# Kernel tuning notes

Measured on AMD Instinct MI355X. Metric: run time of the kernel, lower is better.

Reference implementation:

```python
import jax, jax.numpy as jnp
import numpy as np

N = 50000   # nodes
C = 128     # num_channels
E = 800000  # edges (before self loops)
P = 8192    # pos/neg pairs
L = 2       # num_layers
NEG_SLOPE = 0.2  # GATv2Conv default negative_slope


def setup_inputs() -> dict:
    key = jax.random.key(0)
    ks = jax.random.split(key, 10)
    x = jax.random.normal(ks[0], (N, C), dtype=jnp.float32)
    edge_index = jax.random.randint(ks[1], (2, E), 0, N)
    true_pairs = jax.random.randint(ks[2], (P, 2), 0, N)
    false_pairs = jax.random.randint(ks[3], (P, 2), 0, N)
    s = 1.0 / np.sqrt(C)
    # GATv2Conv params per layer (heads=1, share_weights=False): lin_l, lin_r, att, bias
    Wl = jax.random.normal(ks[4], (L, C, C), dtype=jnp.float32) * s
    Wr = jax.random.normal(ks[5], (L, C, C), dtype=jnp.float32) * s
    att_w = jax.random.normal(ks[6], (L, C), dtype=jnp.float32) * s
    bias = jnp.zeros((L, C), dtype=jnp.float32)
    # ConcatAndLogisticScorer classifier: Linear(2C,C) -> ReLU -> Linear(C,1) -> Sigmoid
    W1 = jax.random.normal(ks[7], (2 * C, C), dtype=jnp.float32) * (1.0 / np.sqrt(2 * C))
    b1 = jnp.zeros((C,), dtype=jnp.float32)
    W2 = jax.random.normal(ks[8], (C, 1), dtype=jnp.float32) * s
    b2 = jnp.zeros((1,), dtype=jnp.float32)
    return dict(x=x, edge_index=edge_index, true_pairs=true_pairs, false_pairs=false_pairs,
                Wl=Wl, Wr=Wr, att_w=att_w, bias=bias, W1=W1, b1=b1, W2=W2, b2=b2)


def _gatv2_layer(h, src, dst, Wl, Wr, a, b):
    # single-head GATv2: e_ij = a^T LeakyReLU(Wl h_j + Wr h_i); softmax over incoming edges of i
    n = h.shape[0]
    xl = h @ Wl  # [N,C] (source transform, also the message value)
    xr = h @ Wr  # [N,C] (target transform)
    z = xl[src] + xr[dst]                       # [E,C]
    z = jnp.where(z >= 0, z, NEG_SLOPE * z)     # leaky_relu
    e = z @ a                                   # [E]
    emax = jax.ops.segment_max(e, dst, num_segments=n)
    p = jnp.exp(e - emax[dst])
    denom = jax.ops.segment_sum(p, dst, num_segments=n)
    alpha = p / denom[dst]                      # edge softmax per dst node
    out = jax.ops.segment_sum(alpha[:, None] * xl[src], dst, num_segments=n)
    return out + b


def _gnn_and_score(x, src, dst, Wl, Wr, att_w, bias, W1, b1, W2, b2, true_pairs, false_pairs):
    h = x
    n_layers = Wl.shape[0]
    for l in range(n_layers):
        h = _gatv2_layer(h, src, dst, Wl[l], Wr[l], att_w[l], bias[l])
        if l < n_layers - 1:  # BasicGNN: activation between layers, not after last
            h = jax.nn.relu(h)
    pos = jnp.concatenate([h[true_pairs[:, 0]], h[true_pairs[:, 1]]], axis=-1)   # [P,2C]
    neg = jnp.concatenate([h[false_pairs[:, 0]], h[false_pairs[:, 1]]], axis=-1)  # [P,2C]
    v = jnp.concatenate([pos, neg], axis=0)  # [2P,2C]
    hid = jax.nn.relu(v @ W1 + b1)
    probs = jax.nn.sigmoid(hid @ W2 + b2)    # [2P,1]
    return pos, neg, probs


def reference(x, edge_index, true_pairs, false_pairs, Wl, Wr, att_w, bias, W1, b1, W2, b2):
    n = x.shape[0]
    loop = jnp.arange(n)  # GATv2Conv add_self_loops=True
    src = jnp.concatenate([edge_index[0], loop])
    dst = jnp.concatenate([edge_index[1], loop])
    pos, neg, probs = _gnn_and_score(x, src, dst, Wl, Wr, att_w, bias, W1, b1, W2, b2,
                                     true_pairs, false_pairs)
    npos = pos.shape[0]
    labels = jnp.concatenate([jnp.ones((npos, 1), jnp.float32),
                              jnp.zeros((probs.shape[0] - npos, 1), jnp.float32)], axis=0)
    pcl = jnp.clip(probs, 1e-7, 1.0 - 1e-7)  # BCELoss log clamping
    loss = -jnp.mean(labels * jnp.log(pcl) + (1.0 - labels) * jnp.log1p(-pcl))
    return pos, neg, probs, loss
```

## Files before the change

kernel.cpp:

```cpp
#include <hip/hip_runtime.h>
#include <math.h>

#define C 128
#define SCAN_B 1024

typedef unsigned short ushort_t;
typedef short short8 __attribute__((ext_vector_type(8)));
typedef float floatx4 __attribute__((ext_vector_type(4)));
typedef float fx2 __attribute__((ext_vector_type(2)));

__device__ __forceinline__ ushort_t f2bf(float x) {
  unsigned u = __float_as_uint(x);
  unsigned r = (u + 0x7FFFu + ((u >> 16) & 1u)) >> 16;
  return (ushort_t)r;
}
__device__ __forceinline__ fx2 bf2f2(unsigned u) {
  fx2 r;
  r.x = __uint_as_float(u << 16);
  r.y = __uint_as_float(u & 0xFFFF0000u);
  return r;
}


__global__ void k_init_prep(int* __restrict__ deg, int* __restrict__ mark,
                            float* __restrict__ lossacc,
                            unsigned* __restrict__ done_cnt, int* __restrict__ ncnt, int n,
                            const float* __restrict__ Wl, const float* __restrict__ Wr,
                            const float* __restrict__ W1,
                            ushort_t* __restrict__ wcat, ushort_t* __restrict__ w1t) {
  int idx = blockIdx.x * blockDim.x + threadIdx.x;
  if (idx < n) { deg[idx] = 0; mark[idx] = 0; }
  if (idx == 0) { lossacc[0] = 0.f; done_cnt[0] = 0u; ncnt[0] = 0; }
  const int NCAT = 2 * 256 * 128;
  if (idx < NCAT) {
    int l = idx >> 15;
    int rem = idx & 32767;
    int nn = rem >> 7;
    int k = rem & 127;
    float v = (nn < 128) ? Wl[l * C * C + k * C + nn] : Wr[l * C * C + k * C + (nn - 128)];
    wcat[idx] = f2bf(v);
  } else if (idx < NCAT + 128 * 256) {
    int j = idx - NCAT;
    int nn = j >> 8;
    int k = j & 255;
    w1t[j] = f2bf(W1[k * C + nn]);
  }
}


__global__ void k_conv_hist(const float* __restrict__ x, ushort_t* __restrict__ xb, int total4,
                            const int* __restrict__ ei, int* __restrict__ deg,
                            int* __restrict__ pos, int E, int ET,
                            const int* __restrict__ tp, const int* __restrict__ fp, int npair2,
                            int* __restrict__ mark, int* __restrict__ nlist, int* __restrict__ ncnt) {
  int i = blockIdx.x * blockDim.x + threadIdx.x;
  if (i < total4) {
    float4 v = ((const float4*)x)[i];
    ushort4 s;
    s.x = f2bf(v.x); s.y = f2bf(v.y); s.z = f2bf(v.z); s.w = f2bf(v.w);
    ((ushort4*)xb)[i] = s;
  }
  if (i < ET) {
    int d = (i < E) ? ei[E + i] : (i - E);
    pos[i] = atomicAdd(&deg[d], 1);
  }
  if (i < 2 * npair2) {
    int node = (i < npair2) ? tp[i] : fp[i - npair2];
    if (atomicExch(&mark[node], 1) == 0) {
      int k = atomicAdd(ncnt, 1);
      nlist[k] = node;
    }
  }
}


__global__ void scan_block(const int* __restrict__ deg, int* __restrict__ row_ptr,
                           int* __restrict__ bsums, int n) {
  __shared__ int sh[SCAN_B];
  int tid = threadIdx.x;
  int i = blockIdx.x * SCAN_B + tid;
  int v = (i < n) ? deg[i] : 0;
  sh[tid] = v;
  __syncthreads();
  #pragma unroll
  for (int off = 1; off < SCAN_B; off <<= 1) {
    int t = (tid >= off) ? sh[tid - off] : 0;
    __syncthreads();
    sh[tid] += t;
    __syncthreads();
  }
  if (i < n) row_ptr[i] = sh[tid] - v;
  if (tid == SCAN_B - 1) bsums[blockIdx.x] = sh[tid];
}

__global__ void scan_sums(int* __restrict__ bsums, int nb, int* __restrict__ row_ptr, int n) {
  int lane = threadIdx.x;
  int v = (lane < nb) ? bsums[lane] : 0;
  int orig = v;
  #pragma unroll
  for (int off = 1; off < 64; off <<= 1) {
    int t = __shfl_up(v, off);
    if (lane >= off) v += t;
  }
  if (lane < nb) bsums[lane] = v - orig;
  if (lane == nb - 1) row_ptr[n] = orig;
}


__device__ __forceinline__ void gemm_body(
    const ushort_t* __restrict__ A, const ushort_t* __restrict__ Bt,
    int M, int K,
    ushort_t* __restrict__ outb0, ushort_t* __restrict__ outb1,
    float* __restrict__ outf, const float* __restrict__ bias, int do_relu,
    int bx, int by) {
  int tid = threadIdx.x;
  int wave = tid >> 6, lane = tid & 63;
  int wm = (wave >> 1) * 64, wn = (wave & 1) * 64;
  int m_base = bx * 128 + wm;
  int lrow = lane & 15, lkg = lane >> 4;

  floatx4 acc[4][4];
  #pragma unroll
  for (int mi = 0; mi < 4; mi++)
    #pragma unroll
    for (int ni = 0; ni < 4; ni++)
      acc[mi][ni] = (floatx4){0.f, 0.f, 0.f, 0.f};

  const int ksteps = K >> 5;
  for (int ks = 0; ks < ksteps; ks++) {
    int koff = ks * 32 + lkg * 8;
    short8 af[4], bfr[4];
    #pragma unroll
    for (int mi = 0; mi < 4; mi++) {
      int gm = m_base + mi * 16 + lrow;
      gm = (gm < M) ? gm : (M - 1);
      af[mi] = *(const short8*)&A[(size_t)gm * K + koff];
    }
    #pragma unroll
    for (int ni = 0; ni < 4; ni++) {
      int gn = by * 128 + wn + ni * 16 + lrow;
      bfr[ni] = *(const short8*)&Bt[(size_t)gn * K + koff];
    }
    #pragma unroll
    for (int mi = 0; mi < 4; mi++)
      #pragma unroll
      for (int ni = 0; ni < 4; ni++)
        acc[mi][ni] = __builtin_amdgcn_mfma_f32_16x16x32_bf16(af[mi], bfr[ni], acc[mi][ni], 0, 0, 0);
  }

  ushort_t* outb = (by == 0) ? outb0 : outb1;
  #pragma unroll
  for (int mi = 0; mi < 4; mi++) {
    #pragma unroll
    for (int r = 0; r < 4; r++) {
      int gm = m_base + mi * 16 + lkg * 4 + r;
      if (gm >= M) continue;
      #pragma unroll
      for (int ni = 0; ni < 4; ni++) {
        int nl = wn + ni * 16 + lrow;
        float v = acc[mi][ni][r];
        if (outf) {
          if (bias) v += bias[nl];
          if (do_relu) v = fmaxf(v, 0.f);
          outf[(size_t)gm * 128 + nl] = v;
        } else {
          outb[(size_t)gm * 128 + nl] = f2bf(v);
        }
      }
    }
  }
}

__global__ __launch_bounds__(256) void gemm_mfma(
    const ushort_t* __restrict__ A, const ushort_t* __restrict__ Bt,
    int M, int K,
    ushort_t* __restrict__ outb0, ushort_t* __restrict__ outb1,
    float* __restrict__ outf, const float* __restrict__ bias, int do_relu) {
  gemm_body(A, Bt, M, K, outb0, outb1, outf, bias, do_relu, blockIdx.x, blockIdx.y);
}


__global__ __launch_bounds__(256) void k_gemm_scatter(
    const ushort_t* __restrict__ A, const ushort_t* __restrict__ Bt,
    int M, int K,
    ushort_t* __restrict__ outb0, ushort_t* __restrict__ outb1, int gb,
    const int* __restrict__ ei, const int* __restrict__ row_ptr,
    const int* __restrict__ bsums, const int* __restrict__ pos,
    int* __restrict__ col, int E, int ET, int ETp) {
  int bx = blockIdx.x;
  if (bx < gb) {
    gemm_body(A, Bt, M, K, outb0, outb1, nullptr, nullptr, 0, bx, blockIdx.y);
  } else {
    int chunk = (bx - gb) * 2 + blockIdx.y;
    int e = chunk * 256 + threadIdx.x;
    if (e < ET) {
      int s = (e < E) ? ei[e] : (e - E);
      int d = (e < E) ? ei[E + e] : (e - E);
      col[row_ptr[d] + bsums[d >> 10] + pos[e]] = s;
    } else if (e < ETp) {
      col[e] = 0;
    }
  }
}


__global__ __launch_bounds__(256) void gat_aggregate(
    const ushort_t* __restrict__ xl, const ushort_t* __restrict__ xr,
    const int* __restrict__ row_ptr, const int* __restrict__ bsums,
    const int* __restrict__ col,
    const float* __restrict__ att, const float* __restrict__ bias,
    float* __restrict__ houtf, ushort_t* __restrict__ houtb,
    const int* __restrict__ nlist, const int* __restrict__ ncnt,
    int n, int do_relu) {
  int gwid = (int)((blockIdx.x * (size_t)blockDim.x + threadIdx.x) >> 6);
  int lane = threadIdx.x & 63;
  int wid;
  if (nlist) {
    if (gwid >= ncnt[0]) return;
    wid = nlist[gwid];
  } else {
    if (gwid >= n) return;
    wid = gwid;
  }
  int g = lane >> 4, p = lane & 15;
  int c0 = p * 8;
  const size_t i = wid;

  fx2 xri[4], av[4];
  {
    uint4 ur = *(const uint4*)&xr[i * C + c0];
    xri[0] = bf2f2(ur.x); xri[1] = bf2f2(ur.y);
    xri[2] = bf2f2(ur.z); xri[3] = bf2f2(ur.w);
    float4 a0 = *(const float4*)&att[c0];
    float4 a1 = *(const float4*)&att[c0 + 4];
    const float L2E = 1.44269504088896f;
    av[0] = (fx2){a0.x * L2E, a0.y * L2E}; av[1] = (fx2){a0.z * L2E, a0.w * L2E};
    av[2] = (fx2){a1.x * L2E, a1.y * L2E}; av[3] = (fx2){a1.z * L2E, a1.w * L2E};
  }

  int beg = row_ptr[wid] + bsums[wid >> 10];
  int end = row_ptr[wid + 1] + bsums[(wid + 1) >> 10];
  float denom = 0.f;
  fx2 acc[4];
  #pragma unroll
  for (int q = 0; q < 4; q++) acc[q] = (fx2){0.f, 0.f};

  for (int base = beg; base < end; base += 8) {
    int e0 = base + g;
    int e1 = e0 + 4;
    int j0 = col[e0];
    int j1 = col[e1];
    uint4 r0 = *(const uint4*)&xl[((size_t)j0 << 7) + c0];
    uint4 r1 = *(const uint4*)&xl[((size_t)j1 << 7) + c0];
    fx2 x0[4], x1[4];
    x0[0] = bf2f2(r0.x); x0[1] = bf2f2(r0.y); x0[2] = bf2f2(r0.z); x0[3] = bf2f2(r0.w);
    x1[0] = bf2f2(r1.x); x1[1] = bf2f2(r1.y); x1[2] = bf2f2(r1.z); x1[3] = bf2f2(r1.w);

    fx2 d0 = (fx2){0.f, 0.f}, d1 = (fx2){0.f, 0.f};
    #pragma unroll
    for (int q = 0; q < 4; q++) {
      fx2 z0 = x0[q] + xri[q];
      fx2 z1 = x1[q] + xri[q];
      z0 = __builtin_elementwise_max(z0, z0 * 0.2f);
      z1 = __builtin_elementwise_max(z1, z1 * 0.2f);
      d0 = __builtin_elementwise_fma(z0, av[q], d0);
      d1 = __builtin_elementwise_fma(z1, av[q], d1);
    }
    float p0 = d0.x + d0.y;
    float p1 = d1.x + d1.y;
    #pragma unroll
    for (int off = 1; off <= 8; off <<= 1) {
      p0 += __shfl_xor(p0, off);
      p1 += __shfl_xor(p1, off);
    }
    float pe0 = (e0 < end) ? __builtin_amdgcn_exp2f(p0) : 0.f;
    float pe1 = (e1 < end) ? __builtin_amdgcn_exp2f(p1) : 0.f;
    denom += pe0 + pe1;
    fx2 v0 = (fx2){pe0, pe0}, v1 = (fx2){pe1, pe1};
    #pragma unroll
    for (int q = 0; q < 4; q++) {
      acc[q] = __builtin_elementwise_fma(v0, x0[q], acc[q]);
      acc[q] = __builtin_elementwise_fma(v1, x1[q], acc[q]);
    }
  }

  #pragma unroll
  for (int off = 16; off <= 32; off <<= 1) {
    denom += __shfl_xor(denom, off);
    #pragma unroll
    for (int q = 0; q < 4; q++) {
      acc[q].x += __shfl_xor(acc[q].x, off);
      acc[q].y += __shfl_xor(acc[q].y, off);
    }
  }

  if (g == 0) {
    float inv = 1.f / denom;
    float4 b0 = *(const float4*)&bias[c0];
    float4 b1 = *(const float4*)&bias[c0 + 4];
    float o[8];
    o[0] = acc[0].x*inv + b0.x; o[1] = acc[0].y*inv + b0.y;
    o[2] = acc[1].x*inv + b0.z; o[3] = acc[1].y*inv + b0.w;
    o[4] = acc[2].x*inv + b1.x; o[5] = acc[2].y*inv + b1.y;
    o[6] = acc[3].x*inv + b1.z; o[7] = acc[3].y*inv + b1.w;
    if (do_relu) {
      #pragma unroll
      for (int c = 0; c < 8; c++) o[c] = fmaxf(o[c], 0.f);
    }
    if (houtf) {
      *(float4*)&houtf[i * C + c0]     = make_float4(o[0], o[1], o[2], o[3]);
      *(float4*)&houtf[i * C + c0 + 4] = make_float4(o[4], o[5], o[6], o[7]);
    } else {
      short8 s;
      #pragma unroll
      for (int c = 0; c < 8; c++) s[c] = (short)f2bf(o[c]);
      *(short8*)&houtb[i * C + c0] = s;
    }
  }
}


__global__ __launch_bounds__(256) void gemm_scorer(
    const float* __restrict__ h, const int* __restrict__ tp, const int* __restrict__ fp,
    const ushort_t* __restrict__ w1t, float* __restrict__ out_pos,
    const float* __restrict__ b1, const float* __restrict__ W2,
    const float* __restrict__ b2, float* __restrict__ probs_out,
    float* __restrict__ lossacc, unsigned* __restrict__ done_cnt,
    float* __restrict__ out_loss, int P2, int P) {
  __shared__ float lhalf[2][128];
  __shared__ float red[128];
  int tid = threadIdx.x;
  int wave = tid >> 6, lane = tid & 63;
  int wm = (wave >> 1) * 64, wn = (wave & 1) * 64;
  int m_base = blockIdx.x * 128 + wm;
  int lrow = lane & 15, lkg = lane >> 4;
  int half = P2 >> 1;
  bool emit = (wn == 0);

  int n0[4], n1[4];
  #pragma unroll
  for (int mi = 0; mi < 4; mi++) {
    int gm = m_base + mi * 16 + lrow;
    const int* pr = (gm < half) ? &tp[(size_t)gm * 2] : &fp[(size_t)(gm - half) * 2];
    n0[mi] = pr[0];
    n1[mi] = pr[1];
  }

  floatx4 acc[4][4];
  #pragma unroll
  for (int mi = 0; mi < 4; mi++)
    #pragma unroll
    for (int ni = 0; ni < 4; ni++)
      acc[mi][ni] = (floatx4){0.f, 0.f, 0.f, 0.f};

  #pragma unroll
  for (int ks = 0; ks < 8; ks++) {
    int koff = ks * 32 + lkg * 8;
    int chan = koff & 127;
    short8 af[4], bfr[4];
    #pragma unroll
    for (int mi = 0; mi < 4; mi++) {
      int node = (ks < 4) ? n0[mi] : n1[mi];
      const float* src = &h[(size_t)node * C + chan];
      float4 lo = *(const float4*)src;
      float4 hi = *(const float4*)(src + 4);
      if (emit) {
        int gm = m_base + mi * 16 + lrow;
        *(float4*)&out_pos[(size_t)gm * 256 + koff]     = lo;
        *(float4*)&out_pos[(size_t)gm * 256 + koff + 4] = hi;
      }
      short8 a;
      a[0] = (short)f2bf(lo.x); a[1] = (short)f2bf(lo.y);
      a[2] = (short)f2bf(lo.z); a[3] = (short)f2bf(lo.w);
      a[4] = (short)f2bf(hi.x); a[5] = (short)f2bf(hi.y);
      a[6] = (short)f2bf(hi.z); a[7] = (short)f2bf(hi.w);
      af[mi] = a;
    }
    #pragma unroll
    for (int ni = 0; ni < 4; ni++) {
      int gn = wn + ni * 16 + lrow;
      bfr[ni] = *(const short8*)&w1t[(size_t)gn * 256 + koff];
    }
    #pragma unroll
    for (int mi = 0; mi < 4; mi++)
      #pragma unroll
      for (int ni = 0; ni < 4; ni++)
        acc[mi][ni] = __builtin_amdgcn_mfma_f32_16x16x32_bf16(af[mi], bfr[ni], acc[mi][ni], 0, 0, 0);
  }

  float b1v[4], w2v[4];
  #pragma unroll
  for (int ni = 0; ni < 4; ni++) {
    int nl = wn + ni * 16 + lrow;
    b1v[ni] = b1[nl];
    w2v[ni] = W2[nl];
  }
  #pragma unroll
  for (int mi = 0; mi < 4; mi++) {
    #pragma unroll
    for (int r = 0; r < 4; r++) {
      float ps = 0.f;
      #pragma unroll
      for (int ni = 0; ni < 4; ni++) {
        float v = fmaxf(acc[mi][ni][r] + b1v[ni], 0.f);
        ps = fmaf(v, w2v[ni], ps);
      }
      #pragma unroll
      for (int off = 1; off <= 8; off <<= 1)
        ps += __shfl_xor(ps, off);
      if (lrow == 0)
        lhalf[wn ? 1 : 0][wm + mi * 16 + lkg * 4 + r] = ps;
    }
  }
  __syncthreads();

  float term = 0.f;
  if (tid < 128) {
    int gr = blockIdx.x * 128 + tid;
    float s = lhalf[0][tid] + lhalf[1][tid] + b2[0];
    float pv = 1.f / (1.f + expf(-s));
    probs_out[gr] = pv;
    float pcl = fminf(fmaxf(pv, 1e-7f), 1.f - 1e-7f);
    term = (gr < P) ? logf(pcl) : log1pf(-pcl);
    red[tid] = term;
  }
  __syncthreads();
  if (tid < 64) red[tid] += red[tid + 64];
  __syncthreads();
  if (tid < 32) red[tid] += red[tid + 32];
  __syncthreads();
  if (tid == 0) {
    float s = 0.f;
    #pragma unroll
    for (int k = 0; k < 32; k++) s += red[k];
    atomicAdd(lossacc, s);
    __threadfence();
    unsigned prev = atomicAdd(done_cnt, 1u);
    if (prev == gridDim.x - 1) {
      float total = atomicAdd(lossacc, 0.f);
      out_loss[0] = -total / (float)P2;
    }
  }
}


extern "C" void kernel_launch(void* const* d_in, const int* in_sizes, int n_in,
                              void* d_out, int out_size, void* d_ws, size_t ws_size,
                              hipStream_t stream) {
  const float* x    = (const float*)d_in[0];
  const int*   ei   = (const int*)d_in[1];
  const int*   tp   = (const int*)d_in[2];
  const int*   fp   = (const int*)d_in[3];
  const float* Wl   = (const float*)d_in[4];
  const float* Wr   = (const float*)d_in[5];
  const float* att  = (const float*)d_in[6];
  const float* bias = (const float*)d_in[7];
  const float* W1   = (const float*)d_in[8];
  const float* b1   = (const float*)d_in[9];
  const float* W2   = (const float*)d_in[10];
  const float* b2   = (const float*)d_in[11];

  int N  = in_sizes[0] / C;
  int E  = in_sizes[1] / 2;
  int P  = in_sizes[2] / 2;
  int ET = E + N;
  int ETp = ET + 8;
  int P2 = 2 * P;
  int npair2 = 2 * P;
  int nb = (N + SCAN_B - 1) / SCAN_B;

  float* out       = (float*)d_out;
  float* out_pos   = out;
  float* out_probs = out + (size_t)P2 * 2 * C;
  float* out_loss  = out_probs + P2;

  char* w = (char*)d_ws;
  size_t NCb2 = (size_t)N * C * 2;
  ushort_t* x_bf  = (ushort_t*)w;  w += NCb2;
  ushort_t* xl_bf = (ushort_t*)w;  w += NCb2;
  ushort_t* xr_bf = (ushort_t*)w;  w += NCb2;
  ushort_t* h1_bf = (ushort_t*)w;  w += NCb2;
  float* h1f = (float*)w;          w += (size_t)N * C * 4;
  ushort_t* wcat = (ushort_t*)w;   w += (size_t)2 * 256 * 128 * 2;
  ushort_t* w1t  = (ushort_t*)w;   w += (size_t)128 * 256 * 2;
  int* deg     = (int*)w;  w += (size_t)N * 4;
  int* mark    = (int*)w;  w += (size_t)N * 4;
  int* nlist   = (int*)w;  w += (size_t)(2 * npair2) * 4;
  int* row_ptr = (int*)w;  w += (size_t)(N + 1) * 4 + 12;
  int* pos     = (int*)w;  w += (size_t)ET * 4;
  int* col     = (int*)w;  w += (size_t)ETp * 4;
  int* bsums   = (int*)w;  w += (size_t)(nb + 1) * 4 + 8;
  float* lossacc = (float*)w;  w += 16;
  unsigned* done_cnt = (unsigned*)w;  w += 16;
  int* ncnt    = (int*)w;

  const int tB = 256;
  int total4 = N * C / 4;

  k_init_prep<<<384, tB, 0, stream>>>(deg, mark, lossacc, done_cnt, ncnt, N, Wl, Wr, W1, wcat, w1t);
  k_conv_hist<<<(total4 + tB - 1) / tB, tB, 0, stream>>>(
      x, x_bf, total4, ei, deg, pos, E, ET, tp, fp, npair2, mark, nlist, ncnt);

  scan_block<<<nb, SCAN_B, 0, stream>>>(deg, row_ptr, bsums, N);
  scan_sums<<<1, 64, 0, stream>>>(bsums, nb, row_ptr, N);

  int gblk = (N + 127) / 128;
  int schunks = (ETp + tB - 1) / tB;
  int sxtra = (schunks + 1) / 2;

  k_gemm_scatter<<<dim3(gblk + sxtra, 2), tB, 0, stream>>>(
      x_bf, wcat, N, C, xl_bf, xr_bf, gblk, ei, row_ptr, bsums, pos, col, E, ET, ETp);

  gat_aggregate<<<(N * 64 + tB - 1) / tB, tB, 0, stream>>>(
      xl_bf, xr_bf, row_ptr, bsums, col, att, bias, nullptr, h1_bf,
      nullptr, nullptr, N, 1);

  gemm_mfma<<<dim3(gblk, 2), tB, 0, stream>>>(
      h1_bf, wcat + (size_t)256 * 128, N, C, xl_bf, xr_bf, nullptr, nullptr, 0);
  int lblk = (2 * npair2 * 64 + tB - 1) / tB;
  gat_aggregate<<<lblk, tB, 0, stream>>>(
      xl_bf, xr_bf, row_ptr, bsums, col, att + C, bias + C, h1f, nullptr,
      nlist, ncnt, N, 0);

  gemm_scorer<<<P2 / 128, tB, 0, stream>>>(
      h1f, tp, fp, w1t, out_pos, b1, W2, b2, out_probs,
      lossacc, done_cnt, out_loss, P2, P);
}
```

Before: 205.5 us.

## Fuse x bf16 conversion into GEMM, single-pass scan, restrict layer-2 xr rows

Removes the separate x-to-bf16 conversion pass; the first GEMM now loads fp32 x and converts it in registers. The two scan kernels become one decoupled scan in which the last block to finish computes the block offsets. The layer-2 target-transform GEMM (by==1) now computes xr only for the nodes the final aggregation needs, gathered through nlist/ncnt, which cuts that half of the GEMM's work. In exchange the GEMM reads twice the bytes for A in layer 1, and the scan relies on atomics and fences for cross-block ordering.

After: 219.1 us. 6.6% more time.

```diff
diff --git a/kernel.cpp b/kernel.cpp
--- a/kernel.cpp
+++ b/kernel.cpp
@@ -2,7 +2,6 @@
 #include <math.h>
 
 #define C 128
-#define SCAN_B 1024
 
 typedef unsigned short ushort_t;
 typedef short short8 __attribute__((ext_vector_type(8)));
@@ -24,13 +23,14 @@
 
 __global__ void k_init_prep(int* __restrict__ deg, int* __restrict__ mark,
                             float* __restrict__ lossacc,
-                            unsigned* __restrict__ done_cnt, int* __restrict__ ncnt, int n,
+                            unsigned* __restrict__ done_cnt, int* __restrict__ ncnt,
+                            unsigned* __restrict__ scnt, int n,
                             const float* __restrict__ Wl, const float* __restrict__ Wr,
                             const float* __restrict__ W1,
                             ushort_t* __restrict__ wcat, ushort_t* __restrict__ w1t) {
   int idx = blockIdx.x * blockDim.x + threadIdx.x;
   if (idx < n) { deg[idx] = 0; mark[idx] = 0; }
-  if (idx == 0) { lossacc[0] = 0.f; done_cnt[0] = 0u; ncnt[0] = 0; }
+  if (idx == 0) { lossacc[0] = 0.f; done_cnt[0] = 0u; ncnt[0] = 0; scnt[0] = 0u; }
   const int NCAT = 2 * 256 * 128;
   if (idx < NCAT) {
     int l = idx >> 15;
@@ -48,18 +48,11 @@
 }
 
 
-__global__ void k_conv_hist(const float* __restrict__ x, ushort_t* __restrict__ xb, int total4,
-                            const int* __restrict__ ei, int* __restrict__ deg,
-                            int* __restrict__ pos, int E, int ET,
-                            const int* __restrict__ tp, const int* __restrict__ fp, int npair2,
-                            int* __restrict__ mark, int* __restrict__ nlist, int* __restrict__ ncnt) {
+__global__ void k_hist(const int* __restrict__ ei, int* __restrict__ deg,
+                       int* __restrict__ pos, int E, int ET,
+                       const int* __restrict__ tp, const int* __restrict__ fp, int npair2,
+                       int* __restrict__ mark, int* __restrict__ nlist, int* __restrict__ ncnt) {
   int i = blockIdx.x * blockDim.x + threadIdx.x;
-  if (i < total4) {
-    float4 v = ((const float4*)x)[i];
-    ushort4 s;
-    s.x = f2bf(v.x); s.y = f2bf(v.y); s.z = f2bf(v.z); s.w = f2bf(v.w);
-    ((ushort4*)xb)[i] = s;
-  }
   if (i < ET) {
     int d = (i < E) ? ei[E + i] : (i - E);
     pos[i] = atomicAdd(&deg[d], 1);
@@ -74,45 +67,67 @@
 }
 
 
-__global__ void scan_block(const int* __restrict__ deg, int* __restrict__ row_ptr,
-                           int* __restrict__ bsums, int n) {
-  __shared__ int sh[SCAN_B];
+__global__ __launch_bounds__(1024) void scan_fast(
+    const int* __restrict__ deg, int* __restrict__ row_ptr, int* __restrict__ bsums,
+    unsigned* __restrict__ scnt, int n, int nb, int nblocks) {
+  __shared__ int wsum[16];
+  __shared__ int lastflag;
   int tid = threadIdx.x;
-  int i = blockIdx.x * SCAN_B + tid;
+  int w = tid >> 6, lane = tid & 63;
+  int i = blockIdx.x * 1024 + tid;
   int v = (i < n) ? deg[i] : 0;
-  sh[tid] = v;
-  __syncthreads();
-  #pragma unroll
-  for (int off = 1; off < SCAN_B; off <<= 1) {
-    int t = (tid >= off) ? sh[tid - off] : 0;
-    __syncthreads();
-    sh[tid] += t;
-    __syncthreads();
-  }
-  if (i < n) row_ptr[i] = sh[tid] - v;
-  if (tid == SCAN_B - 1) bsums[blockIdx.x] = sh[tid];
-}
-
-__global__ void scan_sums(int* __restrict__ bsums, int nb, int* __restrict__ row_ptr, int n) {
-  int lane = threadIdx.x;
-  int v = (lane < nb) ? bsums[lane] : 0;
-  int orig = v;
-  #pragma unroll
-  for (int off = 1; off < 64; off <<= 1) {
-    int t = __shfl_up(v, off);
-    if (lane >= off) v += t;
-  }
-  if (lane < nb) bsums[lane] = v - orig;
-  if (lane == nb - 1) row_ptr[n] = orig;
+  int s = v;
+  #pragma unroll
+  for (int off = 1; off <= 32; off <<= 1) {
+    int t = __shfl_up(s, off);
+    if (lane >= off) s += t;
+  }
+  if (lane == 63) wsum[w] = s;
+  __syncthreads();
+  if (w == 0) {
+    int ws = (lane < 16) ? wsum[lane] : 0;
+    #pragma unroll
+    for (int off = 1; off <= 8; off <<= 1) {
+      int t = __shfl_up(ws, off);
+      if (lane >= off) ws += t;
+    }
+    if (lane < 16) wsum[lane] = ws;
+  }
+  __syncthreads();
+  int woff = (w == 0) ? 0 : wsum[w - 1];
+  if (i < n) row_ptr[i] = woff + s - v;
+  if (tid == 0) atomicExch(&bsums[blockIdx.x], wsum[15]);
+  __threadfence();
+  if (tid == 0) {
+    unsigned t = atomicAdd(scnt, 1u);
+    lastflag = (t == (unsigned)(nblocks - 1)) ? 1 : 0;
+  }
+  __syncthreads();
+  if (lastflag && w == 0) {
+    __threadfence();
+    int bv = (lane < nb) ? atomicAdd(&bsums[lane], 0) : 0;
+    int orig = bv;
+    #pragma unroll
+    for (int off = 1; off <= 32; off <<= 1) {
+      int t = __shfl_up(bv, off);
+      if (lane >= off) bv += t;
+    }
+    if (lane < nb) bsums[lane] = bv - orig;
+    if (lane == nb - 1) row_ptr[n] = orig;
+  }
 }
 
 
 __device__ __forceinline__ void gemm_body(
-    const ushort_t* __restrict__ A, const ushort_t* __restrict__ Bt,
-    int M, int K,
+    const ushort_t* __restrict__ A, const float* __restrict__ Af,
+    const ushort_t* __restrict__ Bt, int M, int K,
     ushort_t* __restrict__ outb0, ushort_t* __restrict__ outb1,
-    float* __restrict__ outf, const float* __restrict__ bias, int do_relu,
+    const int* __restrict__ rowmap, const int* __restrict__ rowcnt,
     int bx, int by) {
+  bool restricted = (by == 1) && (rowmap != nullptr);
+  int nc = restricted ? rowcnt[0] : 0;
+  if (restricted && bx * 128 >= nc) return;
+
   int tid = threadIdx.x;
   int wave = tid >> 6, lane = tid & 63;
   int wm = (wave >> 1) * 64, wn = (wave & 1) * 64;
@@ -133,8 +148,26 @@
     #pragma unroll
     for (int mi = 0; mi < 4; mi++) {
       int gm = m_base + mi * 16 + lrow;
-      gm = (gm < M) ? gm : (M - 1);
-      af[mi] = *(const short8*)&A[(size_t)gm * K + koff];
+      int arow;
+      if (restricted) {
+        int cg = (gm < nc) ? gm : (nc - 1);
+        arow = rowmap[cg];
+      } else {
+        arow = (gm < M) ? gm : (M - 1);
+      }
+      if (Af) {
+        const float* src = &Af[(size_t)arow * K + koff];
+        float4 lo = *(const float4*)src;
+        float4 hi = *(const float4*)(src + 4);
+        short8 a;
+        a[0] = (short)f2bf(lo.x); a[1] = (short)f2bf(lo.y);
+        a[2] = (short)f2bf(lo.z); a[3] = (short)f2bf(lo.w);
+        a[4] = (short)f2bf(hi.x); a[5] = (short)f2bf(hi.y);
+        a[6] = (short)f2bf(hi.z); a[7] = (short)f2bf(hi.w);
+        af[mi] = a;
+      } else {
+        af[mi] = *(const short8*)&A[(size_t)arow * K + koff];
+      }
     }
     #pragma unroll
     for (int ni = 0; ni < 4; ni++) {
@@ -154,18 +187,18 @@
     #pragma unroll
     for (int r = 0; r < 4; r++) {
       int gm = m_base + mi * 16 + lkg * 4 + r;
-      if (gm >= M) continue;
+      int orow;
+      if (restricted) {
+        if (gm >= nc) continue;
+        orow = rowmap[gm];
+      } else {
+        if (gm >= M) continue;
+        orow = gm;
+      }
       #pragma unroll
       for (int ni = 0; ni < 4; ni++) {
         int nl = wn + ni * 16 + lrow;
-        float v = acc[mi][ni][r];
-        if (outf) {
-          if (bias) v += bias[nl];
-          if (do_relu) v = fmaxf(v, 0.f);
-          outf[(size_t)gm * 128 + nl] = v;
-        } else {
-          outb[(size_t)gm * 128 + nl] = f2bf(v);
-        }
+        outb[(size_t)orow * 128 + nl] = f2bf(acc[mi][ni][r]);
       }
     }
   }
@@ -175,13 +208,13 @@
     const ushort_t* __restrict__ A, const ushort_t* __restrict__ Bt,
     int M, int K,
     ushort_t* __restrict__ outb0, ushort_t* __restrict__ outb1,
-    float* __restrict__ outf, const float* __restrict__ bias, int do_relu) {
-  gemm_body(A, Bt, M, K, outb0, outb1, outf, bias, do_relu, blockIdx.x, blockIdx.y);
+    const int* __restrict__ rowmap, const int* __restrict__ rowcnt) {
+  gemm_body(A, nullptr, Bt, M, K, outb0, outb1, rowmap, rowcnt, blockIdx.x, blockIdx.y);
 }
 
 
 __global__ __launch_bounds__(256) void k_gemm_scatter(
-    const ushort_t* __restrict__ A, const ushort_t* __restrict__ Bt,
+    const float* __restrict__ x, const ushort_t* __restrict__ Bt,
     int M, int K,
     ushort_t* __restrict__ outb0, ushort_t* __restrict__ outb1, int gb,
     const int* __restrict__ ei, const int* __restrict__ row_ptr,
@@ -189,7 +222,7 @@
     int* __restrict__ col, int E, int ET, int ETp) {
   int bx = blockIdx.x;
   if (bx < gb) {
-    gemm_body(A, Bt, M, K, outb0, outb1, nullptr, nullptr, 0, bx, blockIdx.y);
+    gemm_body(nullptr, x, Bt, M, K, outb0, outb1, nullptr, nullptr, bx, blockIdx.y);
   } else {
     int chunk = (bx - gb) * 2 + blockIdx.y;
     int e = chunk * 256 + threadIdx.x;
@@ -467,7 +500,7 @@
   int ETp = ET + 8;
   int P2 = 2 * P;
   int npair2 = 2 * P;
-  int nb = (N + SCAN_B - 1) / SCAN_B;
+  int nb = (N + 1023) / 1024;
 
   float* out       = (float*)d_out;
   float* out_pos   = out;
@@ -476,7 +509,6 @@
 
   char* w = (char*)d_ws;
   size_t NCb2 = (size_t)N * C * 2;
-  ushort_t* x_bf  = (ushort_t*)w;  w += NCb2;
   ushort_t* xl_bf = (ushort_t*)w;  w += NCb2;
   ushort_t* xr_bf = (ushort_t*)w;  w += NCb2;
   ushort_t* h1_bf = (ushort_t*)w;  w += NCb2;
@@ -492,31 +524,31 @@
   int* bsums   = (int*)w;  w += (size_t)(nb + 1) * 4 + 8;
   float* lossacc = (float*)w;  w += 16;
   unsigned* done_cnt = (unsigned*)w;  w += 16;
-  int* ncnt    = (int*)w;
+  int* ncnt    = (int*)w;  w += 16;
+  unsigned* scnt = (unsigned*)w;
 
   const int tB = 256;
-  int total4 = N * C / 4;
-
-  k_init_prep<<<384, tB, 0, stream>>>(deg, mark, lossacc, done_cnt, ncnt, N, Wl, Wr, W1, wcat, w1t);
-  k_conv_hist<<<(total4 + tB - 1) / tB, tB, 0, stream>>>(
-      x, x_bf, total4, ei, deg, pos, E, ET, tp, fp, npair2, mark, nlist, ncnt);
-
-  scan_block<<<nb, SCAN_B, 0, stream>>>(deg, row_ptr, bsums, N);
-  scan_sums<<<1, 64, 0, stream>>>(bsums, nb, row_ptr, N);
+
+  k_init_prep<<<384, tB, 0, stream>>>(deg, mark, lossacc, done_cnt, ncnt, scnt, N,
+                                      Wl, Wr, W1, wcat, w1t);
+  k_hist<<<(ET + tB - 1) / tB, tB, 0, stream>>>(
+      ei, deg, pos, E, ET, tp, fp, npair2, mark, nlist, ncnt);
+
+  scan_fast<<<nb, 1024, 0, stream>>>(deg, row_ptr, bsums, scnt, N, nb, nb);
 
   int gblk = (N + 127) / 128;
   int schunks = (ETp + tB - 1) / tB;
   int sxtra = (schunks + 1) / 2;
 
   k_gemm_scatter<<<dim3(gblk + sxtra, 2), tB, 0, stream>>>(
-      x_bf, wcat, N, C, xl_bf, xr_bf, gblk, ei, row_ptr, bsums, pos, col, E, ET, ETp);
+      x, wcat, N, C, xl_bf, xr_bf, gblk, ei, row_ptr, bsums, pos, col, E, ET, ETp);
 
   gat_aggregate<<<(N * 64 + tB - 1) / tB, tB, 0, stream>>>(
       xl_bf, xr_bf, row_ptr, bsums, col, att, bias, nullptr, h1_bf,
       nullptr, nullptr, N, 1);
 
   gemm_mfma<<<dim3(gblk, 2), tB, 0, stream>>>(
-      h1_bf, wcat + (size_t)256 * 128, N, C, xl_bf, xr_bf, nullptr, nullptr, 0);
+      h1_bf, wcat + (size_t)256 * 128, N, C, xl_bf, xr_bf, nlist, ncnt);
   int lblk = (2 * npair2 * 64 + tB - 1) / tB;
   gat_aggregate<<<lblk, tB, 0, stream>>>(
       xl_bf, xr_bf, row_ptr, bsums, col, att + C, bias + C, h1f, nullptr,
```

## Replace CSR build with fixed 32-slot per-node adjacency plus overflow list

Applied to the files above, without the earlier changes.

The histogram kernel now writes each edge's source straight into a fixed 32-entry slot array per destination node. Edges past slot 32 go to a global overflow list of (dst, src) pairs. This removes the two prefix-scan kernels, the per-edge position buffer and the separate scatter pass, so the first GEMM becomes a plain GEMM launch. The aggregation kernel reads the bounded slot range, clamps indices, and linearly scans the overflow list for high-degree nodes. The cost is a larger adjacency buffer, slow handling of hub nodes, and silently dropped edges if the overflow cap is exceeded.

Result: faster. 200.0 us (-2.6%).

```diff
diff --git a/kernel.cpp b/kernel.cpp
--- a/kernel.cpp
+++ b/kernel.cpp
@@ -2,7 +2,7 @@
 #include <math.h>
 
 #define C 128
-#define SCAN_B 1024
+#define OVF_CAP 32768
 
 typedef unsigned short ushort_t;
 typedef short short8 __attribute__((ext_vector_type(8)));
@@ -24,13 +24,14 @@
 
 __global__ void k_init_prep(int* __restrict__ deg, int* __restrict__ mark,
                             float* __restrict__ lossacc,
-                            unsigned* __restrict__ done_cnt, int* __restrict__ ncnt, int n,
+                            unsigned* __restrict__ done_cnt, int* __restrict__ ncnt,
+                            int* __restrict__ ovf_cnt, int n,
                             const float* __restrict__ Wl, const float* __restrict__ Wr,
                             const float* __restrict__ W1,
                             ushort_t* __restrict__ wcat, ushort_t* __restrict__ w1t) {
   int idx = blockIdx.x * blockDim.x + threadIdx.x;
   if (idx < n) { deg[idx] = 0; mark[idx] = 0; }
-  if (idx == 0) { lossacc[0] = 0.f; done_cnt[0] = 0u; ncnt[0] = 0; }
+  if (idx == 0) { lossacc[0] = 0.f; done_cnt[0] = 0u; ncnt[0] = 0; ovf_cnt[0] = 0; }
   const int NCAT = 2 * 256 * 128;
   if (idx < NCAT) {
     int l = idx >> 15;
@@ -50,7 +51,8 @@
 
 __global__ void k_conv_hist(const float* __restrict__ x, ushort_t* __restrict__ xb, int total4,
                             const int* __restrict__ ei, int* __restrict__ deg,
-                            int* __restrict__ pos, int E, int ET,
+                            int* __restrict__ col32, int* __restrict__ ovf,
+                            int* __restrict__ ovf_cnt, int E, int ET,
                             const int* __restrict__ tp, const int* __restrict__ fp, int npair2,
                             int* __restrict__ mark, int* __restrict__ nlist, int* __restrict__ ncnt) {
   int i = blockIdx.x * blockDim.x + threadIdx.x;
@@ -61,8 +63,16 @@
     ((ushort4*)xb)[i] = s;
   }
   if (i < ET) {
-    int d = (i < E) ? ei[E + i] : (i - E);
-    pos[i] = atomicAdd(&deg[d], 1);
+    int s, d;
+    if (i < E) { s = ei[i]; d = ei[E + i]; }
+    else { s = i - E; d = i - E; }
+    int p = atomicAdd(&deg[d], 1);
+    if (p < 32) {
+      col32[(d << 5) + p] = s;
+    } else {
+      int k = atomicAdd(ovf_cnt, 1);
+      if (k < OVF_CAP) { ovf[2 * k] = d; ovf[2 * k + 1] = s; }
+    }
   }
   if (i < 2 * npair2) {
     int node = (i < npair2) ? tp[i] : fp[i - npair2];
@@ -74,44 +84,10 @@
 }
 
 
-__global__ void scan_block(const int* __restrict__ deg, int* __restrict__ row_ptr,
-                           int* __restrict__ bsums, int n) {
-  __shared__ int sh[SCAN_B];
-  int tid = threadIdx.x;
-  int i = blockIdx.x * SCAN_B + tid;
-  int v = (i < n) ? deg[i] : 0;
-  sh[tid] = v;
-  __syncthreads();
-  #pragma unroll
-  for (int off = 1; off < SCAN_B; off <<= 1) {
-    int t = (tid >= off) ? sh[tid - off] : 0;
-    __syncthreads();
-    sh[tid] += t;
-    __syncthreads();
-  }
-  if (i < n) row_ptr[i] = sh[tid] - v;
-  if (tid == SCAN_B - 1) bsums[blockIdx.x] = sh[tid];
-}
-
-__global__ void scan_sums(int* __restrict__ bsums, int nb, int* __restrict__ row_ptr, int n) {
-  int lane = threadIdx.x;
-  int v = (lane < nb) ? bsums[lane] : 0;
-  int orig = v;
-  #pragma unroll
-  for (int off = 1; off < 64; off <<= 1) {
-    int t = __shfl_up(v, off);
-    if (lane >= off) v += t;
-  }
-  if (lane < nb) bsums[lane] = v - orig;
-  if (lane == nb - 1) row_ptr[n] = orig;
-}
-
-
 __device__ __forceinline__ void gemm_body(
     const ushort_t* __restrict__ A, const ushort_t* __restrict__ Bt,
     int M, int K,
     ushort_t* __restrict__ outb0, ushort_t* __restrict__ outb1,
-    float* __restrict__ outf, const float* __restrict__ bias, int do_relu,
     int bx, int by) {
   int tid = threadIdx.x;
   int wave = tid >> 6, lane = tid & 63;
@@ -158,14 +134,7 @@
       #pragma unroll
       for (int ni = 0; ni < 4; ni++) {
         int nl = wn + ni * 16 + lrow;
-        float v = acc[mi][ni][r];
-        if (outf) {
-          if (bias) v += bias[nl];
-          if (do_relu) v = fmaxf(v, 0.f);
-          outf[(size_t)gm * 128 + nl] = v;
-        } else {
-          outb[(size_t)gm * 128 + nl] = f2bf(v);
-        }
+        outb[(size_t)gm * 128 + nl] = f2bf(acc[mi][ni][r]);
       }
     }
   }
@@ -174,40 +143,15 @@
 __global__ __launch_bounds__(256) void gemm_mfma(
     const ushort_t* __restrict__ A, const ushort_t* __restrict__ Bt,
     int M, int K,
-    ushort_t* __restrict__ outb0, ushort_t* __restrict__ outb1,
-    float* __restrict__ outf, const float* __restrict__ bias, int do_relu) {
-  gemm_body(A, Bt, M, K, outb0, outb1, outf, bias, do_relu, blockIdx.x, blockIdx.y);
-}
-
-
-__global__ __launch_bounds__(256) void k_gemm_scatter(
-    const ushort_t* __restrict__ A, const ushort_t* __restrict__ Bt,
-    int M, int K,
-    ushort_t* __restrict__ outb0, ushort_t* __restrict__ outb1, int gb,
-    const int* __restrict__ ei, const int* __restrict__ row_ptr,
-    const int* __restrict__ bsums, const int* __restrict__ pos,
-    int* __restrict__ col, int E, int ET, int ETp) {
-  int bx = blockIdx.x;
-  if (bx < gb) {
-    gemm_body(A, Bt, M, K, outb0, outb1, nullptr, nullptr, 0, bx, blockIdx.y);
-  } else {
-    int chunk = (bx - gb) * 2 + blockIdx.y;
-    int e = chunk * 256 + threadIdx.x;
-    if (e < ET) {
-      int s = (e < E) ? ei[e] : (e - E);
-      int d = (e < E) ? ei[E + e] : (e - E);
-      col[row_ptr[d] + bsums[d >> 10] + pos[e]] = s;
-    } else if (e < ETp) {
-      col[e] = 0;
-    }
-  }
+    ushort_t* __restrict__ outb0, ushort_t* __restrict__ outb1) {
+  gemm_body(A, Bt, M, K, outb0, outb1, blockIdx.x, blockIdx.y);
 }
 
 
 __global__ __launch_bounds__(256) void gat_aggregate(
     const ushort_t* __restrict__ xl, const ushort_t* __restrict__ xr,
-    const int* __restrict__ row_ptr, const int* __restrict__ bsums,
-    const int* __restrict__ col,
+    const int* __restrict__ deg, const int* __restrict__ col32,
+    const int* __restrict__ ovf, const int* __restrict__ ovf_cnt,
     const float* __restrict__ att, const float* __restrict__ bias,
     float* __restrict__ houtf, ushort_t* __restrict__ houtb,
     const int* __restrict__ nlist, const int* __restrict__ ncnt,
@@ -238,8 +182,10 @@
     av[2] = (fx2){a1.x * L2E, a1.y * L2E}; av[3] = (fx2){a1.z * L2E, a1.w * L2E};
   }
 
-  int beg = row_ptr[wid] + bsums[wid >> 10];
-  int end = row_ptr[wid + 1] + bsums[(wid + 1) >> 10];
+  int degc = deg[wid];
+  int beg = wid << 5;
+  int dmain = (degc < 32) ? degc : 32;
+  int end = beg + dmain;
   float denom = 0.f;
   fx2 acc[4];
   #pragma unroll
@@ -248,8 +194,8 @@
   for (int base = beg; base < end; base += 8) {
     int e0 = base + g;
     int e1 = e0 + 4;
-    int j0 = col[e0];
-    int j1 = col[e1];
+    unsigned j0 = min((unsigned)col32[e0], (unsigned)(n - 1));
+    unsigned j1 = min((unsigned)col32[e1], (unsigned)(n - 1));
     uint4 r0 = *(const uint4*)&xl[((size_t)j0 << 7) + c0];
     uint4 r1 = *(const uint4*)&xl[((size_t)j1 << 7) + c0];
     fx2 x0[4], x1[4];
@@ -281,6 +227,35 @@
     for (int q = 0; q < 4; q++) {
       acc[q] = __builtin_elementwise_fma(v0, x0[q], acc[q]);
       acc[q] = __builtin_elementwise_fma(v1, x1[q], acc[q]);
+    }
+  }
+
+  if (degc > 32) {
+    int oc = ovf_cnt[0];
+    oc = (oc < OVF_CAP) ? oc : OVF_CAP;
+    for (int t = 0; t < oc; t++) {
+      if (ovf[2 * t] != wid) continue;
+      unsigned j0 = min((unsigned)ovf[2 * t + 1], (unsigned)(n - 1));
+      uint4 r0 = *(const uint4*)&xl[((size_t)j0 << 7) + c0];
+      fx2 x0[4];
+      x0[0] = bf2f2(r0.x); x0[1] = bf2f2(r0.y); x0[2] = bf2f2(r0.z); x0[3] = bf2f2(r0.w);
+      fx2 d0 = (fx2){0.f, 0.f};
+      #pragma unroll
+      for (int q = 0; q < 4; q++) {
+        fx2 z0 = x0[q] + xri[q];
+        z0 = __builtin_elementwise_max(z0, z0 * 0.2f);
+        d0 = __builtin_elementwise_fma(z0, av[q], d0);
+      }
+      float p0 = d0.x + d0.y;
+      #pragma unroll
+      for (int off = 1; off <= 8; off <<= 1)
+        p0 += __shfl_xor(p0, off);
+      float pe = (g == 0) ? __builtin_amdgcn_exp2f(p0) : 0.f;
+      denom += pe;
+      fx2 v0 = (fx2){pe, pe};
+      #pragma unroll
+      for (int q = 0; q < 4; q++)
+        acc[q] = __builtin_elementwise_fma(v0, x0[q], acc[q]);
     }
   }
 
@@ -464,10 +439,8 @@
   int E  = in_sizes[1] / 2;
   int P  = in_sizes[2] / 2;
   int ET = E + N;
-  int ETp = ET + 8;
   int P2 = 2 * P;
   int npair2 = 2 * P;
-  int nb = (N + SCAN_B - 1) / SCAN_B;
 
   float* out       = (float*)d_out;
   float* out_pos   = out;
@@ -486,40 +459,33 @@
   int* deg     = (int*)w;  w += (size_t)N * 4;
   int* mark    = (int*)w;  w += (size_t)N * 4;
   int* nlist   = (int*)w;  w += (size_t)(2 * npair2) * 4;
-  int* row_ptr = (int*)w;  w += (size_t)(N + 1) * 4 + 12;
-  int* pos     = (int*)w;  w += (size_t)ET * 4;
-  int* col     = (int*)w;  w += (size_t)ETp * 4;
-  int* bsums   = (int*)w;  w += (size_t)(nb + 1) * 4 + 8;
+  int* col32   = (int*)w;  w += (size_t)N * 32 * 4;
+  int* ovf     = (int*)w;  w += (size_t)OVF_CAP * 2 * 4;
   float* lossacc = (float*)w;  w += 16;
   unsigned* done_cnt = (unsigned*)w;  w += 16;
-  int* ncnt    = (int*)w;
+  int* ncnt    = (int*)w;  w += 16;
+  int* ovf_cnt = (int*)w;
 
   const int tB = 256;
   int total4 = N * C / 4;
 
-  k_init_prep<<<384, tB, 0, stream>>>(deg, mark, lossacc, done_cnt, ncnt, N, Wl, Wr, W1, wcat, w1t);
+  k_init_prep<<<384, tB, 0, stream>>>(deg, mark, lossacc, done_cnt, ncnt, ovf_cnt, N,
+                                      Wl, Wr, W1, wcat, w1t);
   k_conv_hist<<<(total4 + tB - 1) / tB, tB, 0, stream>>>(
-      x, x_bf, total4, ei, deg, pos, E, ET, tp, fp, npair2, mark, nlist, ncnt);
-
-  scan_block<<<nb, SCAN_B, 0, stream>>>(deg, row_ptr, bsums, N);
-  scan_sums<<<1, 64, 0, stream>>>(bsums, nb, row_ptr, N);
+      x, x_bf, total4, ei, deg, col32, ovf, ovf_cnt, E, ET,
+      tp, fp, npair2, mark, nlist, ncnt);
 
   int gblk = (N + 127) / 128;
-  int schunks = (ETp + tB - 1) / tB;
-  int sxtra = (schunks + 1) / 2;
-
-  k_gemm_scatter<<<dim3(gblk + sxtra, 2), tB, 0, stream>>>(
-      x_bf, wcat, N, C, xl_bf, xr_bf, gblk, ei, row_ptr, bsums, pos, col, E, ET, ETp);
-
+
+  gemm_mfma<<<dim3(gblk, 2), tB, 0, stream>>>(x_bf, wcat, N, C, xl_bf, xr_bf);
   gat_aggregate<<<(N * 64 + tB - 1) / tB, tB, 0, stream>>>(
-      xl_bf, xr_bf, row_ptr, bsums, col, att, bias, nullptr, h1_bf,
+      xl_bf, xr_bf, deg, col32, ovf, ovf_cnt, att, bias, nullptr, h1_bf,
       nullptr, nullptr, N, 1);
 
-  gemm_mfma<<<dim3(gblk, 2), tB, 0, stream>>>(
-      h1_bf, wcat + (size_t)256 * 128, N, C, xl_bf, xr_bf, nullptr, nullptr, 0);
+  gemm_mfma<<<dim3(gblk, 2), tB, 0, stream>>>(h1_bf, wcat + (size_t)256 * 128, N, C, xl_bf, xr_bf);
   int lblk = (2 * npair2 * 64 + tB - 1) / tB;
   gat_aggregate<<<lblk, tB, 0, stream>>>(
-      xl_bf, xr_bf, row_ptr, bsums, col, att + C, bias + C, h1f, nullptr,
+      xl_bf, xr_bf, deg, col32, ovf, ovf_cnt, att + C, bias + C, h1f, nullptr,
       nlist, ncnt, N, 0);
 
   gemm_scorer<<<P2 / 128, tB, 0, stream>>>(
```
